# Performance work log

Hardware: AMD Instinct MI355X
Metric: run time of the kernel (lower is better)

Reference implementation:

```python
import jax, jax.numpy as jnp
import numpy as np

HIDDEN = 1024
HEADS = 16
HEAD_DIM = HIDDEN // HEADS
SCALE = float(np.sqrt(HEAD_DIM))


def setup_inputs() -> dict:
    key = jax.random.key(0)
    ks = jax.random.split(key, 5)
    x = jax.random.normal(ks[0], (2, 2048, HIDDEN), dtype=jnp.float32)
    # qkv_proj: Linear(hidden, 3*hidden); torch stores weight as [out, in]
    w_qkv = jax.random.normal(ks[1], (3 * HIDDEN, HIDDEN), dtype=jnp.float32) / np.sqrt(HIDDEN)
    b_qkv = jax.random.normal(ks[2], (3 * HIDDEN,), dtype=jnp.float32) * 0.02
    w_out = jax.random.normal(ks[3], (HIDDEN, HIDDEN), dtype=jnp.float32) / np.sqrt(HIDDEN)
    b_out = jax.random.normal(ks[4], (HIDDEN,), dtype=jnp.float32) * 0.02
    return {"x": x, "w_qkv": w_qkv, "b_qkv": b_qkv, "w_out": w_out, "b_out": b_out}


def reference(x, w_qkv, b_qkv, w_out, b_out):
    B, S, H = x.shape
    # fused QKV projection -> [B, S, 3, heads, head_dim]
    qkv = (jnp.einsum('bsh,oh->bso', x, w_qkv) + b_qkv).reshape(B, S, 3, HEADS, HEAD_DIM)
    q, k, v = qkv[:, :, 0], qkv[:, :, 1], qkv[:, :, 2]
    scores = jnp.einsum('bqhd,bkhd->bhqk', q, k) / SCALE
    attn = jax.nn.softmax(scores, axis=-1)  # dropout p=0.0 (eval)
    ctx = jnp.einsum('bhqk,bkhd->bqhd', attn, v).reshape(B, S, H)
    return jnp.einsum('bsh,oh->bso', ctx, w_out) + b_out
```

## Files before the change

### kernel.cpp

```cpp
#include <hip/hip_runtime.h>
#include <math.h>

#define BATCH 2
#define SEQ   2048
#define HIDDEN 1024
#define HEADS 16
#define HD    64
#define QSCALE 0.18033688011112042f

typedef __attribute__((ext_vector_type(8)))  short short8;
typedef __attribute__((ext_vector_type(16))) float f32x16;

__device__ __forceinline__ unsigned short f2bf(float f) {
    unsigned int u = __builtin_bit_cast(unsigned int, f);
    u = (u + 0x7FFFu + ((u >> 16) & 1u)) >> 16;
    return (unsigned short)u;
}
__device__ __forceinline__ unsigned int cvt_pk_bf16(float lo, float hi) {
    unsigned int r;
    asm("v_cvt_pk_bf16_f32 %0, %1, %2" : "=v"(r) : "v"(lo), "v"(hi));
    return r;
}
__device__ __forceinline__ void gl16(const void* g, void* l) {
    __builtin_amdgcn_global_load_lds(
        (const __attribute__((address_space(1))) void*)g,
        (__attribute__((address_space(3))) void*)l,
        16, 0, 0);
}
#define WAIT_VM(N) asm volatile("s_waitcnt vmcnt(" #N ")" ::: "memory")
#define BARRIER()  do { __builtin_amdgcn_s_barrier(); __builtin_amdgcn_sched_barrier(0); } while (0)

__global__ __launch_bounds__(256)
void conv_all(const float* __restrict__ x,  unsigned short* __restrict__ xh,
              const float* __restrict__ wq, unsigned short* __restrict__ wqh,
              const float* __restrict__ wo, unsigned short* __restrict__ woh)
{
    int b = blockIdx.x;
    const float* src;
    unsigned short* dst;
    int base;
    if (b < 4096)      { src = x;  dst = xh;  base = b; }
    else if (b < 7168) { src = wq; dst = wqh; base = b - 4096; }
    else               { src = wo; dst = woh; base = b - 7168; }
    int idx = base * 256 + threadIdx.x;
    float4 v = ((const float4*)src)[idx];
    ushort4 h4;
    h4.x = f2bf(v.x); h4.y = f2bf(v.y); h4.z = f2bf(v.z); h4.w = f2bf(v.w);
    ((ushort4*)dst)[idx] = h4;
}

__device__ __forceinline__ void gemm_core1(
    const char* Ah, const char* Bh,
    int m0, int n0, char* smem, f32x16 acc[2][2])
{
    const int t    = threadIdx.x;
    const int lane = t & 63;
    const int w    = t >> 6;
    const int wm   = w >> 1, wn = w & 1;
    const int l31  = lane & 31, hh = lane >> 5;

    auto stage = [&](int buf, int kt) {
        #pragma unroll
        for (int i = 0; i < 2; ++i) {
            int r  = i * 64 + (t >> 2);
            int cs = (t & 3) ^ ((r >> 1) & 3);
            gl16(Ah + ((size_t)(m0 + r) * 1024 + kt * 32 + cs * 8) * 2,
                 smem + buf * 16384 + i * 4096 + w * 1024);
            gl16(Bh + ((size_t)(n0 + r) * 1024 + kt * 32 + cs * 8) * 2,
                 smem + buf * 16384 + 8192 + i * 4096 + w * 1024);
        }
    };

    stage(0, 0);
    int cur = 0, nxt = 1;
    for (int kt = 0; kt < 32; ++kt) {
        if (kt + 1 < 32) {
            stage(nxt, kt + 1);
            WAIT_VM(4);
        } else {
            WAIT_VM(0);
        }
        BARRIER();
        const char* Ab = smem + cur * 16384;
        const char* Bb = Ab + 8192;
        #pragma unroll
        for (int ks = 0; ks < 2; ++ks) {
            short8 ah[2], bh[2];
            #pragma unroll
            for (int mt = 0; mt < 2; ++mt) {
                int R  = wm * 64 + mt * 32 + l31;
                int ch = ((ks * 2 + hh) ^ ((R >> 1) & 3)) * 16;
                ah[mt] = *(const short8*)(Ab + R * 64 + ch);
            }
            #pragma unroll
            for (int nt = 0; nt < 2; ++nt) {
                int R  = wn * 64 + nt * 32 + l31;
                int ch = ((ks * 2 + hh) ^ ((R >> 1) & 3)) * 16;
                bh[nt] = *(const short8*)(Bb + R * 64 + ch);
            }
            #pragma unroll
            for (int mt = 0; mt < 2; ++mt)
                #pragma unroll
                for (int nt = 0; nt < 2; ++nt)
                    acc[mt][nt] = __builtin_amdgcn_mfma_f32_32x32x16_bf16(ah[mt], bh[nt], acc[mt][nt], 0, 0, 0);
        }
        cur = nxt;
        nxt = (nxt == 2) ? 0 : nxt + 1;
    }
    __syncthreads();
}

__global__ __launch_bounds__(256, 3)
void qkv_gemm(const unsigned short* __restrict__ xh,
              const unsigned short* __restrict__ wh,
              const float* __restrict__ bias,
              unsigned short* __restrict__ qB, unsigned short* __restrict__ kB,
              unsigned short* __restrict__ vtB)
{
    __shared__ __align__(16) char smem[49152];
    f32x16 acc[2][2] = {{{}, {}}, {{}, {}}};
    const int m0 = blockIdx.x * 128, n0 = blockIdx.y * 128;
    gemm_core1((const char*)xh, (const char*)wh, m0, n0, smem, acc);

    const int t    = threadIdx.x;
    const int lane = t & 63;
    const int w    = t >> 6;
    const int wm   = w >> 1, wn = w & 1;
    const int l31  = lane & 31, hh = lane >> 5;

    const int which = n0 >> 10;
    const float scl = (which == 0) ? QSCALE : 1.0f;

    #pragma unroll
    for (int mt = 0; mt < 2; ++mt)
        #pragma unroll
        for (int nt = 0; nt < 2; ++nt) {
            int nl = wn * 64 + nt * 32 + l31;
            float bb = bias[n0 + nl];
            #pragma unroll
            for (int r = 0; r < 16; ++r) {
                int ml = wm * 64 + mt * 32 + (r & 3) + 8 * (r >> 2) + 4 * hh;
                float val = (acc[mt][nt][r] + bb) * scl;
                *(unsigned short*)(smem + ml * 272 + nl * 2) = f2bf(val);
            }
        }
    __syncthreads();

    const int hbase = (n0 & 1023) >> 6;
    const int b     = m0 >> 11;
    const int s0    = m0 & 2047;

    if (which < 2) {
        unsigned short* pp = which ? kB : qB;
        const int nc   = t & 31;
        const int head = hbase + (nc >> 4);
        const int d0   = (nc & 15) * 4;
        #pragma unroll
        for (int it = 0; it < 16; ++it) {
            int m = it * 8 + (t >> 5);
            ushort4 h4 = *(const ushort4*)(smem + m * 272 + nc * 8);
            size_t idx = (((size_t)(b * HEADS + head)) * SEQ + s0 + m) * HD + d0;
            *(ushort4*)&pp[idx] = h4;
        }
    } else {
        const int nl   = t & 127;
        const int head = hbase + (nl >> 6);
        const int d    = nl & 63;
        #pragma unroll
        for (int it = 0; it < 16; ++it) {
            int mq = it * 2 + (t >> 7);
            ushort4 h4;
            h4.x = *(const unsigned short*)(smem + (mq * 4 + 0) * 272 + nl * 2);
            h4.y = *(const unsigned short*)(smem + (mq * 4 + 1) * 272 + nl * 2);
            h4.z = *(const unsigned short*)(smem + (mq * 4 + 2) * 272 + nl * 2);
            h4.w = *(const unsigned short*)(smem + (mq * 4 + 3) * 272 + nl * 2);
            size_t idx = (((size_t)(b * HEADS + head)) * HD + d) * SEQ + s0 + mq * 4;
            *(ushort4*)&vtB[idx] = h4;
        }
    }
}

__global__ __launch_bounds__(256, 3)
void out_gemm(const unsigned short* __restrict__ cth,
              const unsigned short* __restrict__ bh_,
              const float* __restrict__ bias, float* __restrict__ out)
{
    __shared__ __align__(16) char smem[49152];
    f32x16 acc[2][2] = {{{}, {}}, {{}, {}}};
    const int m0 = blockIdx.x * 128, n0 = blockIdx.y * 128;
    gemm_core1((const char*)cth, (const char*)bh_, m0, n0, smem, acc);

    const int t    = threadIdx.x;
    const int lane = t & 63;
    const int w    = t >> 6;
    const int wm   = w >> 1, wn = w & 1;
    const int l31  = lane & 31, hh = lane >> 5;

    #pragma unroll
    for (int mt = 0; mt < 2; ++mt)
        #pragma unroll
        for (int nt = 0; nt < 2; ++nt) {
            int n = n0 + wn * 64 + nt * 32 + l31;
            float bb = bias[n];
            #pragma unroll
            for (int r = 0; r < 16; ++r) {
                int m = m0 + wm * 64 + mt * 32 + (r & 3) + 8 * (r >> 2) + 4 * hh;
                out[(size_t)m * 1024 + n] = acc[mt][nt][r] + bb;
            }
        }
}

#define NPAIR (SEQ / 64)

__global__ __launch_bounds__(512, 4)
void attn_mfma(const unsigned short* __restrict__ qB, const unsigned short* __restrict__ kB,
               const unsigned short* __restrict__ vtB, unsigned short* __restrict__ ctxb)
{
    __shared__ __align__(16) char smem[66048];
    const int t    = threadIdx.x;
    const int lane = t & 63;
    const int wq   = t >> 6;
    const int grp  = wq >> 2;
    const int wql  = wq & 3;
    const int l31  = lane & 31;
    const int hh   = lane >> 5;

    const int bid = blockIdx.x;
    const int xcd = bid & 7, j = bid >> 3;
    const int qt  = j & 15;
    const int bhg = xcd + 8 * (j >> 4);
    const int q0  = qt * 128;
    const size_t bh = (size_t)bhg;

    const char* qP = (const char*)(qB + bh * SEQ * HD);
    const char* kP = (const char*)(kB + bh * SEQ * HD);
    const char* vP = (const char*)(vtB + bh * SEQ * HD);

    const int ringb = grp * 32768;
    const int wb    = wql * 1024;
    const int tg    = t & 255;

    {
        int rr = t >> 3, cc = t & 7;
        #pragma unroll
        for (int i = 0; i < 2; ++i) {
            int row = i * 64 + rr;
            int ch  = cc ^ (row & 7);
            gl16(qP + (size_t)(q0 + row) * 128 + ch * 16,
                 smem + 49152 + i * 8192 + wq * 1024);
        }
    }
    auto stageP = [&](int buf, int p) {
        int base = ringb + buf * 16384;
        int rr = tg >> 3;
        int ch = (tg & 7) ^ (rr & 7);
        gl16(kP + (size_t)(p * 64 + rr) * 128 + ch * 16,      smem + base +     0 + wb);
        gl16(kP + (size_t)(p * 64 + 32 + rr) * 128 + ch * 16, smem + base +  4096 + wb);
        int rr2 = tg >> 2;
        int s4  = (rr2 & 3) ^ ((rr2 >> 2) & 3);
        int ch2 = (tg & 3) ^ s4;
        gl16(vP + (size_t)rr2 * (SEQ * 2) + p * 128 +      ch2 * 16, smem + base +  8192 + wb);
        gl16(vP + (size_t)rr2 * (SEQ * 2) + p * 128 + 64 + ch2 * 16, smem + base + 12288 + wb);
    };
    const int p0 = grp * (NPAIR / 2);
    stageP(0, p0);
    WAIT_VM(4);
    BARRIER();

    short8 qf[4];
    {
        int qrow = 32 * wql + l31;
        #pragma unroll
        for (int ks = 0; ks < 4; ++ks) {
            int ch = ((2 * ks + hh) ^ (qrow & 7)) * 16;
            qf[ks] = *(const short8*)(smem + 49152 + qrow * 128 + ch);
        }
    }
    asm volatile("s_waitcnt lgkmcnt(0)" ::: "memory");
    __builtin_amdgcn_sched_barrier(0);
    BARRIER();

    f32x16 acc0 = {}, acc1 = {};
    float lsum = 0.0f;

    for (int i = 0; i < NPAIR / 2; ++i) {
        if (i + 1 < NPAIR / 2) { stageP((i + 1) & 1, p0 + i + 1); WAIT_VM(4); }
        else                   { WAIT_VM(0); }
        BARRIER();

        const char* Pb = smem + ringb + (i & 1) * 16384;

        f32x16 sa = {}, sb = {};
        __builtin_amdgcn_s_setprio(1);
        #pragma unroll
        for (int ks = 0; ks < 4; ++ks) {
            int ch = ((2 * ks + hh) ^ (l31 & 7)) * 16;
            short8 ka = *(const short8*)(Pb +        l31 * 128 + ch);
            short8 kb = *(const short8*)(Pb + 4096 + l31 * 128 + ch);
            sa = __builtin_amdgcn_mfma_f32_32x32x16_bf16(ka, qf[ks], sa, 0, 0, 0);
            sb = __builtin_amdgcn_mfma_f32_32x32x16_bf16(kb, qf[ks], sb, 0, 0, 0);
        }
        __builtin_amdgcn_s_setprio(0);

        unsigned int pa_[8], pb_[8];
        float ps0 = 0.f, ps1 = 0.f, ps2 = 0.f, ps3 = 0.f;
        #pragma unroll
        for (int w = 0; w < 8; ++w) {
            float e0 = __builtin_amdgcn_exp2f(sa[2 * w]);
            float e1 = __builtin_amdgcn_exp2f(sa[2 * w + 1]);
            ps0 += e0; ps1 += e1;
            pa_[w] = cvt_pk_bf16(e0, e1);
            float f0 = __builtin_amdgcn_exp2f(sb[2 * w]);
            float f1 = __builtin_amdgcn_exp2f(sb[2 * w + 1]);
            ps2 += f0; ps3 += f1;
            pb_[w] = cvt_pk_bf16(f0, f1);
        }
        lsum += (ps0 + ps1) + (ps2 + ps3);

        const char* Va = Pb + 8192;
        const char* Vb = Pb + 12288;
        __builtin_amdgcn_s_setprio(1);
        #pragma unroll
        for (int ks = 0; ks < 2; ++ks) {
            unsigned int a0 = pa_[4*ks],     a2 = pa_[4*ks + 2];
            unsigned int a1 = pa_[4*ks + 1], a3 = pa_[4*ks + 3];
            asm volatile("v_permlane32_swap_b32 %0, %1" : "+v"(a0), "+v"(a2));
            asm volatile("v_permlane32_swap_b32 %0, %1" : "+v"(a1), "+v"(a3));
            unsigned int b0 = pb_[4*ks],     b2 = pb_[4*ks + 2];
            unsigned int b1 = pb_[4*ks + 1], b3 = pb_[4*ks + 3];
            asm volatile("v_permlane32_swap_b32 %0, %1" : "+v"(b0), "+v"(b2));
            asm volatile("v_permlane32_swap_b32 %0, %1" : "+v"(b1), "+v"(b3));
            short8 pA = __builtin_bit_cast(short8, make_uint4(a0, a1, a2, a3));
            short8 pB = __builtin_bit_cast(short8, make_uint4(b0, b1, b2, b3));
            #pragma unroll
            for (int mt = 0; mt < 2; ++mt) {
                int rrow = 32 * mt + l31;
                int s4   = (rrow & 3) ^ ((rrow >> 2) & 3);
                int ch   = ((2 * ks + hh) ^ s4) * 16;
                short8 va = *(const short8*)(Va + rrow * 64 + ch);
                short8 vb = *(const short8*)(Vb + rrow * 64 + ch);
                if (mt == 0) {
                    acc0 = __builtin_amdgcn_mfma_f32_32x32x16_bf16(va, pA, acc0, 0, 0, 0);
                    acc0 = __builtin_amdgcn_mfma_f32_32x32x16_bf16(vb, pB, acc0, 0, 0, 0);
                } else {
                    acc1 = __builtin_amdgcn_mfma_f32_32x32x16_bf16(va, pA, acc1, 0, 0, 0);
                    acc1 = __builtin_amdgcn_mfma_f32_32x32x16_bf16(vb, pB, acc1, 0, 0, 0);
                }
            }
        }
        __builtin_amdgcn_s_setprio(0);
        BARRIER();
    }

    lsum += __shfl_xor(lsum, 32, 64);
    __syncthreads();
    const int qrow = 32 * wql + l31;
    if (grp == 1) {
        int idx = t - 256;
        #pragma unroll
        for (int m2 = 0; m2 < 4; ++m2) {
            *(float4*)(smem + 16384 + (m2 * 256 + idx) * 16) =
                make_float4(acc0[4*m2+0], acc0[4*m2+1], acc0[4*m2+2], acc0[4*m2+3]);
            *(float4*)(smem + 16384 + ((m2 + 4) * 256 + idx) * 16) =
                make_float4(acc1[4*m2+0], acc1[4*m2+1], acc1[4*m2+2], acc1[4*m2+3]);
        }
        if (hh == 0) ((float*)(smem + 65536))[qrow] = lsum;
    }
    __syncthreads();
    if (grp == 0) {
        float l1 = ((float*)(smem + 65536))[qrow];
        float inv = 1.0f / (lsum + l1);
        #pragma unroll
        for (int m2 = 0; m2 < 4; ++m2) {
            float4 pa = *(const float4*)(smem + 16384 + (m2 * 256 + t) * 16);
            float4 pb = *(const float4*)(smem + 16384 + ((m2 + 4) * 256 + t) * 16);
            ushort4 h4a, h4b;
            h4a.x = f2bf((acc0[4*m2+0] + pa.x) * inv);
            h4a.y = f2bf((acc0[4*m2+1] + pa.y) * inv);
            h4a.z = f2bf((acc0[4*m2+2] + pa.z) * inv);
            h4a.w = f2bf((acc0[4*m2+3] + pa.w) * inv);
            h4b.x = f2bf((acc1[4*m2+0] + pb.x) * inv);
            h4b.y = f2bf((acc1[4*m2+1] + pb.y) * inv);
            h4b.z = f2bf((acc1[4*m2+2] + pb.z) * inv);
            h4b.w = f2bf((acc1[4*m2+3] + pb.w) * inv);
            int d0a = 4 * hh + 8 * m2;
            int ca  = (d0a >> 3) ^ (qrow & 7);
            *(ushort4*)(smem + qrow * 128 + ca * 16 + (d0a & 7) * 2) = h4a;
            int d0b = 4 * hh + 8 * m2 + 32;
            int cb  = (d0b >> 3) ^ (qrow & 7);
            *(ushort4*)(smem + qrow * 128 + cb * 16 + (d0b & 7) * 2) = h4b;
        }
    }
    __syncthreads();
    {
        #pragma unroll
        for (int it = 0; it < 2; ++it) {
            int slot = it * 512 + t;
            int row  = slot >> 3;
            int p    = slot & 7;
            uint4 v4 = *(const uint4*)(smem + row * 128 + ((p ^ (row & 7)) * 16));
            *(uint4*)&ctxb[((size_t)(bhg >> 4) * SEQ + q0 + row) * HIDDEN
                           + (bhg & 15) * HD + p * 8] = v4;
        }
    }
}

extern "C" void kernel_launch(void* const* d_in, const int* in_sizes, int n_in,
                              void* d_out, int out_size, void* d_ws, size_t ws_size,
                              hipStream_t stream)
{
    const float* x     = (const float*)d_in[0];
    const float* w_qkv = (const float*)d_in[1];
    const float* b_qkv = (const float*)d_in[2];
    const float* w_out = (const float*)d_in[3];
    const float* b_out = (const float*)d_in[4];
    float* out = (float*)d_out;

    const size_t PH = (size_t)BATCH * HEADS * SEQ * HD;
    unsigned short* ws = (unsigned short*)d_ws;
    unsigned short* qB  = ws;
    unsigned short* kB  = ws + PH;
    unsigned short* vtB = ws + 2 * PH;
    unsigned short* wqh = ws + 3 * PH;
    unsigned short* woh = wqh + 3 * PH / 4;
    unsigned short* cth = woh + PH / 4;
    unsigned short* xh  = (unsigned short*)d_out;

    conv_all<<<8192, 256, 0, stream>>>(x, xh, w_qkv, wqh, w_out, woh);
    qkv_gemm<<<dim3(32, 24), 256, 0, stream>>>(xh, wqh, b_qkv, qB, kB, vtB);
    attn_mfma<<<512, 512, 0, stream>>>(qB, kB, vtB, cth);
    out_gemm<<<dim3(32, 8), 256, 0, stream>>>(cth, woh, b_out, out);
}
```

Before: 107.8 us.

## Shrink attention blocks to 64 query rows and 32-key tiles per stage

The attention kernel is retiled from 512-thread blocks covering 128 query rows with 64-key stages to 256-thread blocks covering 64 query rows with 32-key stages, doubling the grid to 1024 blocks. Shared memory is halved, and each wave now does one QK and one PV MFMA chain per stage instead of two. This aims to raise occupancy and block-level parallelism, at the cost of more K/V reloads across blocks, twice as many barriers per key range, and less MFMA work per synchronisation.

```diff
diff --git a/kernel.cpp b/kernel.cpp
--- a/kernel.cpp
+++ b/kernel.cpp
@@ -210,70 +210,72 @@
         }
 }
 
-#define NPAIR (SEQ / 64)
-
-__global__ __launch_bounds__(512, 4)
+#define NT 32
+
+__global__ __launch_bounds__(256, 4)
 void attn_mfma(const unsigned short* __restrict__ qB, const unsigned short* __restrict__ kB,
                const unsigned short* __restrict__ vtB, unsigned short* __restrict__ ctxb)
 {
-    __shared__ __align__(16) char smem[66048];
+    __shared__ __align__(16) char smem[33024];
     const int t    = threadIdx.x;
     const int lane = t & 63;
     const int wq   = t >> 6;
-    const int grp  = wq >> 2;
-    const int wql  = wq & 3;
+    const int grp  = wq >> 1;
+    const int wg   = wq & 1;
     const int l31  = lane & 31;
     const int hh   = lane >> 5;
+    const int tg   = t & 127;
 
     const int bid = blockIdx.x;
     const int xcd = bid & 7, j = bid >> 3;
-    const int qt  = j & 15;
-    const int bhg = xcd + 8 * (j >> 4);
-    const int q0  = qt * 128;
+    const int qt  = j & 31;
+    const int bhg = xcd + 8 * (j >> 5);
+    const int q0  = qt * 64;
     const size_t bh = (size_t)bhg;
 
     const char* qP = (const char*)(qB + bh * SEQ * HD);
     const char* kP = (const char*)(kB + bh * SEQ * HD);
     const char* vP = (const char*)(vtB + bh * SEQ * HD);
 
-    const int ringb = grp * 32768;
-    const int wb    = wql * 1024;
-    const int tg    = t & 255;
-
     {
-        int rr = t >> 3, cc = t & 7;
         #pragma unroll
         for (int i = 0; i < 2; ++i) {
-            int row = i * 64 + rr;
-            int ch  = cc ^ (row & 7);
+            int row = i * 32 + (t >> 3);
+            int ch  = (t & 7) ^ (row & 7);
             gl16(qP + (size_t)(q0 + row) * 128 + ch * 16,
-                 smem + 49152 + i * 8192 + wq * 1024);
-        }
-    }
-    auto stageP = [&](int buf, int p) {
-        int base = ringb + buf * 16384;
-        int rr = tg >> 3;
-        int ch = (tg & 7) ^ (rr & 7);
-        gl16(kP + (size_t)(p * 64 + rr) * 128 + ch * 16,      smem + base +     0 + wb);
-        gl16(kP + (size_t)(p * 64 + 32 + rr) * 128 + ch * 16, smem + base +  4096 + wb);
-        int rr2 = tg >> 2;
-        int s4  = (rr2 & 3) ^ ((rr2 >> 2) & 3);
-        int ch2 = (tg & 3) ^ s4;
-        gl16(vP + (size_t)rr2 * (SEQ * 2) + p * 128 +      ch2 * 16, smem + base +  8192 + wb);
-        gl16(vP + (size_t)rr2 * (SEQ * 2) + p * 128 + 64 + ch2 * 16, smem + base + 12288 + wb);
+                 smem + 24576 + i * 4096 + wq * 1024);
+        }
+    }
+    auto stageT = [&](int buf, int gkt) {
+        int base = (grp * 2 + buf) * 8192;
+        #pragma unroll
+        for (int j2 = 0; j2 < 2; ++j2) {
+            int rr = j2 * 16 + (tg >> 3);
+            int ch = (tg & 7) ^ (rr & 7);
+            gl16(kP + (size_t)(gkt * 32 + rr) * 128 + ch * 16,
+                 smem + base + j2 * 2048 + wg * 1024);
+        }
+        #pragma unroll
+        for (int j2 = 0; j2 < 2; ++j2) {
+            int r  = j2 * 32 + (tg >> 2);
+            int s4 = (r & 3) ^ ((r >> 2) & 3);
+            int ch = (tg & 3) ^ s4;
+            gl16(vP + (size_t)r * (SEQ * 2) + gkt * 64 + ch * 16,
+                 smem + base + 4096 + j2 * 2048 + wg * 1024);
+        }
     };
-    const int p0 = grp * (NPAIR / 2);
-    stageP(0, p0);
+    const int gk0 = grp * NT;
+    stageT(0, gk0);
     WAIT_VM(4);
     BARRIER();
 
     short8 qf[4];
     {
-        int qrow = 32 * wql + l31;
+        int qrow = 32 * wg + l31;
         #pragma unroll
         for (int ks = 0; ks < 4; ++ks) {
             int ch = ((2 * ks + hh) ^ (qrow & 7)) * 16;
-            qf[ks] = *(const short8*)(smem + 49152 + qrow * 128 + ch);
+            qf[ks] = *(const short8*)(smem + 24576 + qrow * 128 + ch);
         }
     }
     asm volatile("s_waitcnt lgkmcnt(0)" ::: "memory");
@@ -283,42 +285,35 @@
     f32x16 acc0 = {}, acc1 = {};
     float lsum = 0.0f;
 
-    for (int i = 0; i < NPAIR / 2; ++i) {
-        if (i + 1 < NPAIR / 2) { stageP((i + 1) & 1, p0 + i + 1); WAIT_VM(4); }
-        else                   { WAIT_VM(0); }
+    for (int i = 0; i < NT; ++i) {
+        if (i + 1 < NT) { stageT((i + 1) & 1, gk0 + i + 1); WAIT_VM(2); }
+        else            { WAIT_VM(0); }
         BARRIER();
 
-        const char* Pb = smem + ringb + (i & 1) * 16384;
-
-        f32x16 sa = {}, sb = {};
+        const char* Kb = smem + (grp * 2 + (i & 1)) * 8192;
+
+        f32x16 sacc = {};
         __builtin_amdgcn_s_setprio(1);
         #pragma unroll
         for (int ks = 0; ks < 4; ++ks) {
             int ch = ((2 * ks + hh) ^ (l31 & 7)) * 16;
-            short8 ka = *(const short8*)(Pb +        l31 * 128 + ch);
-            short8 kb = *(const short8*)(Pb + 4096 + l31 * 128 + ch);
-            sa = __builtin_amdgcn_mfma_f32_32x32x16_bf16(ka, qf[ks], sa, 0, 0, 0);
-            sb = __builtin_amdgcn_mfma_f32_32x32x16_bf16(kb, qf[ks], sb, 0, 0, 0);
+            short8 ka = *(const short8*)(Kb + l31 * 128 + ch);
+            sacc = __builtin_amdgcn_mfma_f32_32x32x16_bf16(ka, qf[ks], sacc, 0, 0, 0);
         }
         __builtin_amdgcn_s_setprio(0);
 
-        unsigned int pa_[8], pb_[8];
-        float ps0 = 0.f, ps1 = 0.f, ps2 = 0.f, ps3 = 0.f;
+        unsigned int pa_[8];
+        float ps0 = 0.f, ps1 = 0.f;
         #pragma unroll
         for (int w = 0; w < 8; ++w) {
-            float e0 = __builtin_amdgcn_exp2f(sa[2 * w]);
-            float e1 = __builtin_amdgcn_exp2f(sa[2 * w + 1]);
+            float e0 = __builtin_amdgcn_exp2f(sacc[2 * w]);
+            float e1 = __builtin_amdgcn_exp2f(sacc[2 * w + 1]);
             ps0 += e0; ps1 += e1;
             pa_[w] = cvt_pk_bf16(e0, e1);
-            float f0 = __builtin_amdgcn_exp2f(sb[2 * w]);
-            float f1 = __builtin_amdgcn_exp2f(sb[2 * w + 1]);
-            ps2 += f0; ps3 += f1;
-            pb_[w] = cvt_pk_bf16(f0, f1);
-        }
-        lsum += (ps0 + ps1) + (ps2 + ps3);
-
-        const char* Va = Pb + 8192;
-        const char* Vb = Pb + 12288;
+        }
+        lsum += ps0 + ps1;
+
+        const char* Vb = Kb + 4096;
         __builtin_amdgcn_s_setprio(1);
         #pragma unroll
         for (int ks = 0; ks < 2; ++ks) {
@@ -326,26 +321,17 @@
             unsigned int a1 = pa_[4*ks + 1], a3 = pa_[4*ks + 3];
             asm volatile("v_permlane32_swap_b32 %0, %1" : "+v"(a0), "+v"(a2));
             asm volatile("v_permlane32_swap_b32 %0, %1" : "+v"(a1), "+v"(a3));
-            unsigned int b0 = pb_[4*ks],     b2 = pb_[4*ks + 2];
-            unsigned int b1 = pb_[4*ks + 1], b3 = pb_[4*ks + 3];
-            asm volatile("v_permlane32_swap_b32 %0, %1" : "+v"(b0), "+v"(b2));
-            asm volatile("v_permlane32_swap_b32 %0, %1" : "+v"(b1), "+v"(b3));
             short8 pA = __builtin_bit_cast(short8, make_uint4(a0, a1, a2, a3));
-            short8 pB = __builtin_bit_cast(short8, make_uint4(b0, b1, b2, b3));
             #pragma unroll
             for (int mt = 0; mt < 2; ++mt) {
                 int rrow = 32 * mt + l31;
                 int s4   = (rrow & 3) ^ ((rrow >> 2) & 3);
                 int ch   = ((2 * ks + hh) ^ s4) * 16;
-                short8 va = *(const short8*)(Va + rrow * 64 + ch);
-                short8 vb = *(const short8*)(Vb + rrow * 64 + ch);
-                if (mt == 0) {
+                short8 va = *(const short8*)(Vb + rrow * 64 + ch);
+                if (mt == 0)
                     acc0 = __builtin_amdgcn_mfma_f32_32x32x16_bf16(va, pA, acc0, 0, 0, 0);
-                    acc0 = __builtin_amdgcn_mfma_f32_32x32x16_bf16(vb, pB, acc0, 0, 0, 0);
-                } else {
+                else
                     acc1 = __builtin_amdgcn_mfma_f32_32x32x16_bf16(va, pA, acc1, 0, 0, 0);
-                    acc1 = __builtin_amdgcn_mfma_f32_32x32x16_bf16(vb, pB, acc1, 0, 0, 0);
-                }
             }
         }
         __builtin_amdgcn_s_setprio(0);
@@ -354,26 +340,26 @@
 
     lsum += __shfl_xor(lsum, 32, 64);
     __syncthreads();
-    const int qrow = 32 * wql + l31;
+    const int qrow = 32 * wg + l31;
     if (grp == 1) {
-        int idx = t - 256;
+        int idx = t - 128;
         #pragma unroll
         for (int m2 = 0; m2 < 4; ++m2) {
-            *(float4*)(smem + 16384 + (m2 * 256 + idx) * 16) =
+            *(float4*)(smem + (m2 * 128 + idx) * 16) =
                 make_float4(acc0[4*m2+0], acc0[4*m2+1], acc0[4*m2+2], acc0[4*m2+3]);
-            *(float4*)(smem + 16384 + ((m2 + 4) * 256 + idx) * 16) =
+            *(float4*)(smem + 8192 + (m2 * 128 + idx) * 16) =
                 make_float4(acc1[4*m2+0], acc1[4*m2+1], acc1[4*m2+2], acc1[4*m2+3]);
         }
-        if (hh == 0) ((float*)(smem + 65536))[qrow] = lsum;
+        if (hh == 0) ((float*)(smem + 32768))[qrow] = lsum;
     }
     __syncthreads();
     if (grp == 0) {
-        float l1 = ((float*)(smem + 65536))[qrow];
+        float l1 = ((float*)(smem + 32768))[qrow];
         float inv = 1.0f / (lsum + l1);
         #pragma unroll
         for (int m2 = 0; m2 < 4; ++m2) {
-            float4 pa = *(const float4*)(smem + 16384 + (m2 * 256 + t) * 16);
-            float4 pb = *(const float4*)(smem + 16384 + ((m2 + 4) * 256 + t) * 16);
+            float4 pa = *(const float4*)(smem + (m2 * 128 + t) * 16);
+            float4 pb = *(const float4*)(smem + 8192 + (m2 * 128 + t) * 16);
             ushort4 h4a, h4b;
             h4a.x = f2bf((acc0[4*m2+0] + pa.x) * inv);
             h4a.y = f2bf((acc0[4*m2+1] + pa.y) * inv);
@@ -385,20 +371,20 @@
             h4b.w = f2bf((acc1[4*m2+3] + pb.w) * inv);
             int d0a = 4 * hh + 8 * m2;
             int ca  = (d0a >> 3) ^ (qrow & 7);
-            *(ushort4*)(smem + qrow * 128 + ca * 16 + (d0a & 7) * 2) = h4a;
+            *(ushort4*)(smem + 16384 + qrow * 128 + ca * 16 + (d0a & 7) * 2) = h4a;
             int d0b = 4 * hh + 8 * m2 + 32;
             int cb  = (d0b >> 3) ^ (qrow & 7);
-            *(ushort4*)(smem + qrow * 128 + cb * 16 + (d0b & 7) * 2) = h4b;
+            *(ushort4*)(smem + 16384 + qrow * 128 + cb * 16 + (d0b & 7) * 2) = h4b;
         }
     }
     __syncthreads();
     {
         #pragma unroll
         for (int it = 0; it < 2; ++it) {
-            int slot = it * 512 + t;
+            int slot = it * 256 + t;
             int row  = slot >> 3;
             int p    = slot & 7;
-            uint4 v4 = *(const uint4*)(smem + row * 128 + ((p ^ (row & 7)) * 16));
+            uint4 v4 = *(const uint4*)(smem + 16384 + row * 128 + ((p ^ (row & 7)) * 16));
             *(uint4*)&ctxb[((size_t)(bhg >> 4) * SEQ + q0 + row) * HIDDEN
                            + (bhg & 15) * HD + p * 8] = v4;
         }
@@ -428,6 +414,6 @@
 
     conv_all<<<8192, 256, 0, stream>>>(x, xh, w_qkv, wqh, w_out, woh);
     qkv_gemm<<<dim3(32, 24), 256, 0, stream>>>(xh, wqh, b_qkv, qB, kB, vtB);
-    attn_mfma<<<512, 512, 0, stream>>>(qB, kB, vtB, cth);
+    attn_mfma<<<1024, 256, 0, stream>>>(qB, kB, vtB, cth);
     out_gemm<<<dim3(32, 8), 256, 0, stream>>>(cth, woh, b_out, out);
 }
```

Result: slower. 116.2 us (+7.8%).
